# Kernel tuning notes

Measured on AMD Instinct MI355X. Metric: run time of the kernel, lower is better.

The kernel has to match this reference:

```python
import jax, jax.numpy as jnp
import numpy as np
from jax import lax

HEADS = 8
DIM_HEAD = 8
SCALE = DIM_HEAD ** (-0.5)
UP = 64  # nn.Upsample(scale_factor=64), nearest


def _conv_s8(x, w, b):
    # Conv2d(inner, inner, 11x11, stride 8, padding 2) + exact GELU
    y = lax.conv_general_dilated(x, w, window_strides=(8, 8),
                                 padding=((2, 2), (2, 2)),
                                 dimension_numbers=('NCHW', 'OIHW', 'NCHW'))
    return jax.nn.gelu(y + b[None, :, None, None], approximate=False)


def setup_inputs() -> dict:
    key = jax.random.key(0)
    ks = jax.random.split(key, 8)
    b, c, h, w = 2, 64, 48, 48
    inner = HEADS * DIM_HEAD  # 64
    f = jax.random.normal(ks[0], (b, c, h, w), jnp.float32)
    w_qkv = jax.random.normal(ks[1], (inner * 3, c, 1, 1), jnp.float32) * 0.05
    wq = jax.random.normal(ks[2], (inner, inner, 11, 11), jnp.float32) * 0.02
    bq = jax.random.normal(ks[3], (inner,), jnp.float32) * 0.02
    wk = jax.random.normal(ks[4], (inner, inner, 11, 11), jnp.float32) * 0.02
    bk = jax.random.normal(ks[5], (inner,), jnp.float32) * 0.02
    pos_h = jax.random.normal(ks[6], (DIM_HEAD, h), jnp.float32) * SCALE
    pos_w = jax.random.normal(ks[7], (DIM_HEAD, w), jnp.float32) * SCALE
    return {"f": f, "w_qkv": w_qkv, "wq": wq, "bq": bq, "wk": wk,
            "bk": bk, "pos_h": pos_h, "pos_w": pos_w}


def reference(f, w_qkv, wq, bq, wk, bk, pos_h, pos_w):
    b, c, h, w = f.shape
    inner = HEADS * DIM_HEAD
    # 1x1 conv to qkv
    qkv = jnp.einsum('oc,bchw->bohw', w_qkv[:, :, 0, 0], f)
    q, k, v = jnp.split(qkv, 3, axis=1)  # each [b, inner, h, w]
    # positional logits from pre-conv q
    q_full = q.reshape(b, HEADS, DIM_HEAD, h * w)
    emb = (pos_h[:, :, None] + pos_w[:, None, :]).reshape(DIM_HEAD, h * w)
    pos_logits = jnp.einsum('bhci,cj->bhij', q_full, emb)  # [b,H,hw,hw]
    # strided conv + gelu on q,k
    qd = _conv_s8(q, wq, bq)
    kd = _conv_s8(k, wk, bk)
    m = qd.shape[-1]  # downsampled side
    qd = qd.reshape(b, HEADS, DIM_HEAD, m * m) * SCALE
    kd = kd.reshape(b, HEADS, DIM_HEAD, m * m)
    vv = v.reshape(b, HEADS, DIM_HEAD, h * w)
    dots = jnp.einsum('bhci,bhcj->bhij', qd, kd)  # [b,H,m^2,m^2]
    # nearest upsample x64 on last two dims
    dots = jnp.repeat(jnp.repeat(dots, UP, axis=-2), UP, axis=-1)
    attn = jax.nn.softmax(dots + pos_logits, axis=-1)
    fmap = jnp.einsum('bhij,bhcj->bhci', attn, vv)
    return fmap.reshape(b, inner, h, w)
```

## Files before the change

kernel.cpp:

```cpp
#include <hip/hip_runtime.h>
#include <math.h>

#define HW 2304
#define O192 192
#define SCALE_F 0.35355339059327373f

typedef unsigned int u32;
typedef __attribute__((address_space(1))) const u32 gu32;
typedef __attribute__((address_space(3))) u32 lu32;
__device__ __forceinline__ void dma16(const void* g, void* l) {
  __builtin_amdgcn_global_load_lds((gu32*)g, (lu32*)l, 16, 0, 0);
}

__global__ __launch_bounds__(256) void qkv_kernel(
    const float* __restrict__ F, const float* __restrict__ W,
    float* __restrict__ QKV, float* __restrict__ V2) {
  __shared__ __align__(16) float sW[384];
  int blk = blockIdx.x;
  int idx0 = blk * 256;
  int r0 = idx0 / HW;
  int r1 = (idx0 + 255) / HW;
  int tid = threadIdx.x;
  if (tid < 192) {
    int g = tid >> 6, c = tid & 63;
    sW[tid]       = W[((r0 & 63) + g * 64) * 64 + c];
    sW[192 + tid] = W[((r1 & 63) + g * 64) * 64 + c];
  }
  __syncthreads();
  int idx = idx0 + tid;
  int p  = idx % HW;
  int r  = idx / HW;
  int o0 = r & 63;
  int b  = r >> 6;
  const float4* w4 = (const float4*)(sW + ((r == r0) ? 0 : 192));
  const float* f = F + (b * 64) * HW + p;
  float aq = 0.f, ak = 0.f, av = 0.f;
  #pragma unroll 4
  for (int c4 = 0; c4 < 16; c4++) {
    float4 wq = w4[c4];
    float4 wk = w4[16 + c4];
    float4 wv = w4[32 + c4];
    float f0 = f[(c4 * 4 + 0) * HW];
    float f1 = f[(c4 * 4 + 1) * HW];
    float f2 = f[(c4 * 4 + 2) * HW];
    float f3 = f[(c4 * 4 + 3) * HW];
    aq = fmaf(wq.x, f0, aq); ak = fmaf(wk.x, f0, ak); av = fmaf(wv.x, f0, av);
    aq = fmaf(wq.y, f1, aq); ak = fmaf(wk.y, f1, ak); av = fmaf(wv.y, f1, av);
    aq = fmaf(wq.z, f2, aq); ak = fmaf(wk.z, f2, ak); av = fmaf(wv.z, f2, av);
    aq = fmaf(wq.w, f3, aq); ak = fmaf(wk.w, f3, ak); av = fmaf(wv.w, f3, av);
  }
  float* qp = QKV + (b * HW + p) * O192;
  qp[o0]      = aq;
  qp[o0 + 64] = ak;
  V2[(((b << 3) + (o0 >> 3)) * HW + p) * 8 + (o0 & 7)] = av;
}

__global__ __launch_bounds__(256) void conv_kernel(
    const float* __restrict__ QKV, const float* __restrict__ Wq,
    const float* __restrict__ Bq, const float* __restrict__ Wk,
    const float* __restrict__ Bk, float* __restrict__ QD) {
  __shared__ float sW[7744];
  __shared__ float sRed[4 * 64 * 6];
  int blk = blockIdx.x;
  int xcd = blk & 7;
  int T = xcd >> 2, b = (xcd >> 1) & 1, s = xcd & 1;
  int idx = (blk >> 3) * 2 + s;
  int o  = idx / 6;
  int oy = idx % 6;
  const float* Wg = T ? Wk : Wq;
  for (int i = threadIdx.x; i < 7744; i += 256) sW[i] = Wg[o * 7744 + i];
  __syncthreads();
  int wv = threadIdx.x >> 6;
  int c  = threadIdx.x & 63;
  const float* base = QKV + b * (HW * O192) + T * 64 + c;
  float acc[6];
  #pragma unroll
  for (int ox = 0; ox < 6; ox++) acc[ox] = 0.f;
  for (int kyi = 0; kyi < 3; kyi++) {
    int ky = wv * 3 + kyi;
    if (ky > 10) break;
    int y = oy * 8 - 2 + ky;
    if ((unsigned)y < 48u) {
      float xrow[48];
      #pragma unroll
      for (int x = 0; x < 48; x++) xrow[x] = base[(y * 48 + x) * O192];
      #pragma unroll
      for (int kx = 0; kx < 11; kx++) {
        float wt = sW[c * 121 + ky * 11 + kx];
        #pragma unroll
        for (int ox = 0; ox < 6; ox++) {
          int x = ox * 8 - 2 + kx;
          if (x >= 0 && x < 48) acc[ox] = fmaf(xrow[x], wt, acc[ox]);
        }
      }
    }
  }
  #pragma unroll
  for (int ox = 0; ox < 6; ox++) sRed[(wv * 64 + c) * 6 + ox] = acc[ox];
  __syncthreads();
  if (threadIdx.x < 64) {
    int t = threadIdx.x;
    float r[6];
    #pragma unroll
    for (int ox = 0; ox < 6; ox++)
      r[ox] = sRed[t * 6 + ox] + sRed[(64 + t) * 6 + ox]
            + sRed[(128 + t) * 6 + ox] + sRed[(192 + t) * 6 + ox];
    #pragma unroll
    for (int off = 32; off; off >>= 1) {
      #pragma unroll
      for (int ox = 0; ox < 6; ox++) r[ox] += __shfl_down(r[ox], off, 64);
    }
    if (t == 0) {
      float bias = T ? Bk[o] : Bq[o];
      #pragma unroll
      for (int ox = 0; ox < 6; ox++) {
        float g = r[ox] + bias;
        float ge = 0.5f * g * (1.0f + erff(g * 0.70710678118654752f));
        QD[((T * 2 + b) * 64 + o) * 36 + oy * 6 + ox] = ge;
      }
    }
  }
}

#define OFF_V   0
#define OFF_EA  4608
#define OFF_PHT 7680
#define OFF_PWT 8064
#define OFF_E4  8448
#define OFF_U   8592
#define SBUF_N  11152

__global__ __launch_bounds__(512, 4) void attn_kernel(
    const float* __restrict__ QKV, const float* __restrict__ V2,
    const float* __restrict__ QD, const float* __restrict__ PH,
    const float* __restrict__ PW, float* __restrict__ Pnum,
    float* __restrict__ PZ) {
  __shared__ __align__(16) float sB[SBUF_N];
  int blk = blockIdx.x;
  int bh = blk / 36;
  int rem = blk - bh * 36;
  int q = rem & 3, S = rem >> 2;
  int b = bh >> 3, h = bh & 7;
  int tid = threadIdx.x;
  int w = tid >> 6, lane = tid & 63;
  int l32 = lane & 31, chalf = lane >> 5;
  if (tid < 384) {
    sB[OFF_PHT + tid] = PH[(tid & 7) * 48 + (tid >> 3)];
    sB[OFF_PWT + tid] = PW[(tid & 7) * 48 + (tid >> 3)];
  }
  if (tid < 144) {
    int J = tid >> 2, k4 = tid & 3;
    const float* qd = QD + ((0 + b) * 64 + h * 8) * 36 + (S * 4 + k4);
    const float* kd = QD + ((2 + b) * 64 + h * 8) * 36 + J;
    float acc = 0.f;
    #pragma unroll
    for (int c8 = 0; c8 < 8; c8++) acc = fmaf(qd[c8 * 36], kd[c8 * 36], acc);
    sB[OFF_E4 + J * 4 + k4] = __expf(SCALE_F * acc);
  }
  {
    int row = tid >> 1, half = tid & 1;
    *(float4*)(sB + OFF_U + tid * 4) =
      *(const float4*)(QKV + (b * HW + S * 256 + row) * O192 + h * 8 + half * 4);
  }
  {
    const char* src = (const char*)(V2 + (size_t)bh * (HW * 8) + q * 4608);
    for (int m = w; m < 18; m += 8)
      dma16(src + m * 1024 + lane * 16, (char*)(sB + OFF_V) + m * 1024);
  }
  __syncthreads();
  #pragma unroll
  for (int m = 0; m < 6; m++) {
    int flat = tid + m * 512;
    int jyL = flat >> 8, row = flat & 255;
    const float* qp = sB + OFF_U + row * 8;
    const float* pp = sB + OFF_PHT + (q * 12 + jyL) * 8;
    float d = qp[0]*pp[0]+qp[1]*pp[1]+qp[2]*pp[2]+qp[3]*pp[3]
            + qp[4]*pp[4]+qp[5]*pp[5]+qp[6]*pp[6]+qp[7]*pp[7];
    sB[OFF_EA + jyL * 256 + (row & 31) * 8 + (row >> 5)] = __expf(d);
  }
  float pw[6][8];
  #pragma unroll
  for (int i = 0; i < 6; i++) {
    float4 a = *(const float4*)(sB + OFF_PWT + (w * 6 + i) * 8);
    float4 c = *(const float4*)(sB + OFF_PWT + (w * 6 + i) * 8 + 4);
    pw[i][0]=a.x; pw[i][1]=a.y; pw[i][2]=a.z; pw[i][3]=a.w;
    pw[i][4]=c.x; pw[i][5]=c.y; pw[i][6]=c.z; pw[i][7]=c.w;
  }
  float eB[8][6];
  #pragma unroll
  for (int k8 = 0; k8 < 8; k8++) {
    const float* qp = sB + OFF_U + (k8 * 32 + l32) * 8;
    float4 qa = *(const float4*)qp;
    float4 qb = *(const float4*)(qp + 4);
    #pragma unroll
    for (int i = 0; i < 6; i++) {
      float d = qa.x*pw[i][0]+qa.y*pw[i][1]+qa.z*pw[i][2]+qa.w*pw[i][3]
              + qb.x*pw[i][4]+qb.y*pw[i][5]+qb.z*pw[i][6]+qb.w*pw[i][7];
      eB[k8][i] = __expf(d);
    }
  }
  float accv[8][4], zz[8];
  #pragma unroll
  for (int k8 = 0; k8 < 8; k8++) {
    zz[k8] = 0.f;
    #pragma unroll
    for (int c = 0; c < 4; c++) accv[k8][c] = 0.f;
  }
  __syncthreads();
  const float4* sV4 = (const float4*)(sB + OFF_V);
  for (int jyL = 0; jyL < 12; jyL++) {
    float4 ea0 = *(const float4*)(sB + OFF_EA + jyL * 256 + l32 * 8);
    float4 ea1 = *(const float4*)(sB + OFF_EA + jyL * 256 + l32 * 8 + 4);
    int cb = (q * 12 + jyL) * 48 + w * 6;
    int J0 = cb >> 6, J1 = (cb + 5) >> 6;
    int ib = 64 - (cb & 63);
    float4 e0 = *(const float4*)(sB + OFF_E4 + J0 * 4);
    float4 e1 = *(const float4*)(sB + OFF_E4 + J1 * 4);
    float a0[8], a1[8];
    a0[0]=ea0.x*e0.x; a0[1]=ea0.y*e0.x; a0[2]=ea0.z*e0.y; a0[3]=ea0.w*e0.y;
    a0[4]=ea1.x*e0.z; a0[5]=ea1.y*e0.z; a0[6]=ea1.z*e0.w; a0[7]=ea1.w*e0.w;
    a1[0]=ea0.x*e1.x; a1[1]=ea0.y*e1.x; a1[2]=ea0.z*e1.y; a1[3]=ea0.w*e1.y;
    a1[4]=ea1.x*e1.z; a1[5]=ea1.y*e1.z; a1[6]=ea1.z*e1.w; a1[7]=ea1.w*e1.w;
    #pragma unroll
    for (int i = 0; i < 6; i++) {
      float4 v = sV4[(jyL * 48 + w * 6 + i) * 2 + chalf];
      bool s0 = (i < ib);
      #pragma unroll
      for (int k8 = 0; k8 < 8; k8++) {
        float wgt = (s0 ? a0[k8] : a1[k8]) * eB[k8][i];
        accv[k8][0] = fmaf(wgt, v.x, accv[k8][0]);
        accv[k8][1] = fmaf(wgt, v.y, accv[k8][1]);
        accv[k8][2] = fmaf(wgt, v.z, accv[k8][2]);
        accv[k8][3] = fmaf(wgt, v.w, accv[k8][3]);
        zz[k8] += wgt;
      }
    }
  }
  float* sU = sB + OFF_U;
  #pragma unroll
  for (int k8 = 0; k8 < 8; k8++) {
    __syncthreads();
    {
      float* rp = sU + (w * 64 + lane) * 5;
      rp[0] = accv[k8][0]; rp[1] = accv[k8][1];
      rp[2] = accv[k8][2]; rp[3] = accv[k8][3];
      rp[4] = zz[k8];
    }
    __syncthreads();
    if (tid < 256) {
      int row32 = tid & 31, c = tid >> 5;
      int ln = row32 + (c >> 2) * 32;
      float num = 0.f;
      #pragma unroll
      for (int ww = 0; ww < 8; ww++) num += sU[(ww * 64 + ln) * 5 + (c & 3)];
      Pnum[((q * 16 + bh) * 8 + c) * HW + S * 256 + k8 * 32 + row32] = num;
    } else if (tid < 288) {
      int row32 = tid & 31;
      float z = 0.f;
      #pragma unroll
      for (int ww = 0; ww < 8; ww++)
        z += sU[(ww * 64 + row32) * 5 + 4] + sU[(ww * 64 + 32 + row32) * 5 + 4];
      PZ[(q * 16 + bh) * HW + S * 256 + k8 * 32 + row32] = z * 0.5f;
    }
  }
}

__global__ __launch_bounds__(256) void combine_kernel(
    const float* __restrict__ Pnum, const float* __restrict__ PZ,
    float* __restrict__ out) {
  int t = blockIdx.x * 256 + threadIdx.x;
  int row = t % HW;
  int rc = t / HW;
  int c = rc & 7, bh = rc >> 3;
  float num = 0.f, z = 0.f;
  #pragma unroll
  for (int q = 0; q < 4; q++) {
    num += Pnum[((q * 16 + bh) * 8 + c) * HW + row];
    z   += PZ[(q * 16 + bh) * HW + row];
  }
  int b = bh >> 3, h = bh & 7;
  out[(b * 64 + h * 8 + c) * HW + row] = num / z;
}

extern "C" void kernel_launch(void* const* d_in, const int* in_sizes, int n_in,
                              void* d_out, int out_size, void* d_ws, size_t ws_size,
                              hipStream_t stream) {
  const float* F    = (const float*)d_in[0];
  const float* Wqkv = (const float*)d_in[1];
  const float* Wq   = (const float*)d_in[2];
  const float* Bq   = (const float*)d_in[3];
  const float* Wk   = (const float*)d_in[4];
  const float* Bk   = (const float*)d_in[5];
  const float* PH   = (const float*)d_in[6];
  const float* PW   = (const float*)d_in[7];
  float* out = (float*)d_out;

  float* ws   = (float*)d_ws;
  float* QKV  = ws;
  float* V2   = QKV + 2 * HW * O192;
  float* QD   = V2 + 2 * 8 * HW * 8;
  float* Pnum = QD + 2 * 2 * 64 * 36;
  float* PZ   = Pnum + 4 * 16 * 8 * HW;

  qkv_kernel    <<<1152, 256, 0, stream>>>(F, Wqkv, QKV, V2);
  conv_kernel   <<<1536, 256, 0, stream>>>(QKV, Wq, Bq, Wk, Bk, QD);
  attn_kernel   <<<576,  512, 0, stream>>>(QKV, V2, QD, PH, PW, Pnum, PZ);
  combine_kernel<<<1152, 256, 0, stream>>>(Pnum, PZ, out);
}
```

Before: 159.5 us.

## Fuse combine into attention kernel by looping over all key quarters per block

Each attention block now covers 128 query rows across all four key quarters, streaming the V quarters through shared memory in a loop. This removes the Pnum/PZ partial buffers and the separate combine kernel, so normalization is written directly to the output. In exchange the grid shrinks from 576 to 288 blocks with fewer query rows per block, which lowers parallelism on the GPU. The V loads are now serialized between barriers with no double buffering.

```diff
diff --git a/kernel.cpp b/kernel.cpp
--- a/kernel.cpp
+++ b/kernel.cpp
@@ -122,25 +122,26 @@
   }
 }
 
-#define OFF_V   0
-#define OFF_EA  4608
-#define OFF_PHT 7680
-#define OFF_PWT 8064
-#define OFF_E4  8448
-#define OFF_U   8592
-#define SBUF_N  11152
-
-__global__ __launch_bounds__(512, 4) void attn_kernel(
+#define OFF_V    0
+#define OFF_QLO  4608
+#define OFF_QHI  5120
+#define OFF_EA   5632
+#define OFF_PHT  11776
+#define OFF_PWT  12160
+#define OFF_E    12544
+#define OFF_Z    12616
+#define SBUF_N   12648
+
+__global__ __launch_bounds__(512) void attn_kernel(
     const float* __restrict__ QKV, const float* __restrict__ V2,
     const float* __restrict__ QD, const float* __restrict__ PH,
-    const float* __restrict__ PW, float* __restrict__ Pnum,
-    float* __restrict__ PZ) {
+    const float* __restrict__ PW, float* __restrict__ out) {
   __shared__ __align__(16) float sB[SBUF_N];
   int blk = blockIdx.x;
-  int bh = blk / 36;
-  int rem = blk - bh * 36;
-  int q = rem & 3, S = rem >> 2;
+  int bh = blk & 15;
+  int Ip = blk >> 4;
   int b = bh >> 3, h = bh & 7;
+  int r0 = Ip * 128;
   int tid = threadIdx.x;
   int w = tid >> 6, lane = tid & 63;
   int l32 = lane & 31, chalf = lane >> 5;
@@ -148,97 +149,95 @@
     sB[OFF_PHT + tid] = PH[(tid & 7) * 48 + (tid >> 3)];
     sB[OFF_PWT + tid] = PW[(tid & 7) * 48 + (tid >> 3)];
   }
-  if (tid < 144) {
-    int J = tid >> 2, k4 = tid & 3;
-    const float* qd = QD + ((0 + b) * 64 + h * 8) * 36 + (S * 4 + k4);
+  if (tid < 72) {
+    int Ik = tid / 36, J = tid - Ik * 36;
+    const float* qd = QD + ((0 + b) * 64 + h * 8) * 36 + (Ip * 2 + Ik);
     const float* kd = QD + ((2 + b) * 64 + h * 8) * 36 + J;
     float acc = 0.f;
     #pragma unroll
     for (int c8 = 0; c8 < 8; c8++) acc = fmaf(qd[c8 * 36], kd[c8 * 36], acc);
-    sB[OFF_E4 + J * 4 + k4] = __expf(SCALE_F * acc);
-  }
-  {
+    sB[OFF_E + tid] = __expf(SCALE_F * acc);
+  }
+  if (tid < 256) {
     int row = tid >> 1, half = tid & 1;
-    *(float4*)(sB + OFF_U + tid * 4) =
-      *(const float4*)(QKV + (b * HW + S * 256 + row) * O192 + h * 8 + half * 4);
-  }
-  {
-    const char* src = (const char*)(V2 + (size_t)bh * (HW * 8) + q * 4608);
-    for (int m = w; m < 18; m += 8)
-      dma16(src + m * 1024 + lane * 16, (char*)(sB + OFF_V) + m * 1024);
-  }
-  __syncthreads();
-  #pragma unroll
-  for (int m = 0; m < 6; m++) {
+    int slot = (row & 31) * 4 + (row >> 5);
+    float4 qv = *(const float4*)(QKV + (b * HW + r0 + row) * O192 + h * 8 + half * 4);
+    *(float4*)(sB + (half ? OFF_QHI : OFF_QLO) + slot * 4) = qv;
+  }
+  __syncthreads();
+  #pragma unroll
+  for (int m = 0; m < 12; m++) {
     int flat = tid + m * 512;
-    int jyL = flat >> 8, row = flat & 255;
-    const float* qp = sB + OFF_U + row * 8;
-    const float* pp = sB + OFF_PHT + (q * 12 + jyL) * 8;
-    float d = qp[0]*pp[0]+qp[1]*pp[1]+qp[2]*pp[2]+qp[3]*pp[3]
-            + qp[4]*pp[4]+qp[5]*pp[5]+qp[6]*pp[6]+qp[7]*pp[7];
-    sB[OFF_EA + jyL * 256 + (row & 31) * 8 + (row >> 5)] = __expf(d);
-  }
-  float pw[6][8];
-  #pragma unroll
-  for (int i = 0; i < 6; i++) {
-    float4 a = *(const float4*)(sB + OFF_PWT + (w * 6 + i) * 8);
-    float4 c = *(const float4*)(sB + OFF_PWT + (w * 6 + i) * 8 + 4);
-    pw[i][0]=a.x; pw[i][1]=a.y; pw[i][2]=a.z; pw[i][3]=a.w;
-    pw[i][4]=c.x; pw[i][5]=c.y; pw[i][6]=c.z; pw[i][7]=c.w;
-  }
-  float eB[8][6];
-  #pragma unroll
-  for (int k8 = 0; k8 < 8; k8++) {
-    const float* qp = sB + OFF_U + (k8 * 32 + l32) * 8;
-    float4 qa = *(const float4*)qp;
-    float4 qb = *(const float4*)(qp + 4);
+    int jy = flat >> 7, s = flat & 127;
+    float4 qa = *(const float4*)(sB + OFF_QLO + s * 4);
+    float4 qb = *(const float4*)(sB + OFF_QHI + s * 4);
+    const float* pp = sB + OFF_PHT + jy * 8;
+    float d = qa.x*pp[0]+qa.y*pp[1]+qa.z*pp[2]+qa.w*pp[3]
+            + qb.x*pp[4]+qb.y*pp[5]+qb.z*pp[6]+qb.w*pp[7];
+    sB[OFF_EA + flat] = __expf(d);
+  }
+  float eB[4][6];
+  #pragma unroll
+  for (int k8 = 0; k8 < 4; k8++) {
+    float4 qa = *(const float4*)(sB + OFF_QLO + (l32 * 4 + k8) * 4);
+    float4 qb = *(const float4*)(sB + OFF_QHI + (l32 * 4 + k8) * 4);
     #pragma unroll
     for (int i = 0; i < 6; i++) {
-      float d = qa.x*pw[i][0]+qa.y*pw[i][1]+qa.z*pw[i][2]+qa.w*pw[i][3]
-              + qb.x*pw[i][4]+qb.y*pw[i][5]+qb.z*pw[i][6]+qb.w*pw[i][7];
+      const float* pp = sB + OFF_PWT + (w * 6 + i) * 8;
+      float d = qa.x*pp[0]+qa.y*pp[1]+qa.z*pp[2]+qa.w*pp[3]
+              + qb.x*pp[4]+qb.y*pp[5]+qb.z*pp[6]+qb.w*pp[7];
       eB[k8][i] = __expf(d);
     }
   }
-  float accv[8][4], zz[8];
-  #pragma unroll
-  for (int k8 = 0; k8 < 8; k8++) {
+  float accv[4][4], zz[4];
+  #pragma unroll
+  for (int k8 = 0; k8 < 4; k8++) {
     zz[k8] = 0.f;
     #pragma unroll
     for (int c = 0; c < 4; c++) accv[k8][c] = 0.f;
   }
-  __syncthreads();
   const float4* sV4 = (const float4*)(sB + OFF_V);
-  for (int jyL = 0; jyL < 12; jyL++) {
-    float4 ea0 = *(const float4*)(sB + OFF_EA + jyL * 256 + l32 * 8);
-    float4 ea1 = *(const float4*)(sB + OFF_EA + jyL * 256 + l32 * 8 + 4);
-    int cb = (q * 12 + jyL) * 48 + w * 6;
-    int J0 = cb >> 6, J1 = (cb + 5) >> 6;
-    int ib = 64 - (cb & 63);
-    float4 e0 = *(const float4*)(sB + OFF_E4 + J0 * 4);
-    float4 e1 = *(const float4*)(sB + OFF_E4 + J1 * 4);
-    float a0[8], a1[8];
-    a0[0]=ea0.x*e0.x; a0[1]=ea0.y*e0.x; a0[2]=ea0.z*e0.y; a0[3]=ea0.w*e0.y;
-    a0[4]=ea1.x*e0.z; a0[5]=ea1.y*e0.z; a0[6]=ea1.z*e0.w; a0[7]=ea1.w*e0.w;
-    a1[0]=ea0.x*e1.x; a1[1]=ea0.y*e1.x; a1[2]=ea0.z*e1.y; a1[3]=ea0.w*e1.y;
-    a1[4]=ea1.x*e1.z; a1[5]=ea1.y*e1.z; a1[6]=ea1.z*e1.w; a1[7]=ea1.w*e1.w;
-    #pragma unroll
-    for (int i = 0; i < 6; i++) {
-      float4 v = sV4[(jyL * 48 + w * 6 + i) * 2 + chalf];
-      bool s0 = (i < ib);
-      #pragma unroll
-      for (int k8 = 0; k8 < 8; k8++) {
-        float wgt = (s0 ? a0[k8] : a1[k8]) * eB[k8][i];
-        accv[k8][0] = fmaf(wgt, v.x, accv[k8][0]);
-        accv[k8][1] = fmaf(wgt, v.y, accv[k8][1]);
-        accv[k8][2] = fmaf(wgt, v.z, accv[k8][2]);
-        accv[k8][3] = fmaf(wgt, v.w, accv[k8][3]);
-        zz[k8] += wgt;
+  for (int p = 0; p < 4; p++) {
+    __syncthreads();
+    {
+      const char* src = (const char*)(V2 + (size_t)bh * (HW * 8) + p * 4608);
+      for (int m = w; m < 18; m += 8)
+        dma16(src + m * 1024 + lane * 16, (char*)(sB + OFF_V) + m * 1024);
+    }
+    __syncthreads();
+    #pragma unroll
+    for (int jyL = 0; jyL < 12; jyL++) {
+      int jy = p * 12 + jyL;
+      float4 ea = *(const float4*)(sB + OFF_EA + jy * 128 + l32 * 4);
+      int cb = jy * 48 + w * 6;
+      int J0 = cb >> 6, J1 = (cb + 5) >> 6;
+      int ib = 64 - (cb & 63);
+      float e00 = sB[OFF_E + J0], e01 = sB[OFF_E + 36 + J0];
+      float e10 = sB[OFF_E + J1], e11 = sB[OFF_E + 36 + J1];
+      float a0[4], a1[4];
+      a0[0] = ea.x * e00; a0[1] = ea.y * e00;
+      a0[2] = ea.z * e01; a0[3] = ea.w * e01;
+      a1[0] = ea.x * e10; a1[1] = ea.y * e10;
+      a1[2] = ea.z * e11; a1[3] = ea.w * e11;
+      #pragma unroll
+      for (int i = 0; i < 6; i++) {
+        float4 v = sV4[(jyL * 48 + w * 6 + i) * 2 + chalf];
+        bool s0 = (i < ib);
+        #pragma unroll
+        for (int k8 = 0; k8 < 4; k8++) {
+          float wgt = (s0 ? a0[k8] : a1[k8]) * eB[k8][i];
+          accv[k8][0] = fmaf(wgt, v.x, accv[k8][0]);
+          accv[k8][1] = fmaf(wgt, v.y, accv[k8][1]);
+          accv[k8][2] = fmaf(wgt, v.z, accv[k8][2]);
+          accv[k8][3] = fmaf(wgt, v.w, accv[k8][3]);
+          zz[k8] += wgt;
+        }
       }
     }
   }
-  float* sU = sB + OFF_U;
-  #pragma unroll
-  for (int k8 = 0; k8 < 8; k8++) {
+  float* sU = sB + OFF_EA;
+  #pragma unroll
+  for (int k8 = 0; k8 < 4; k8++) {
     __syncthreads();
     {
       float* rp = sU + (w * 64 + lane) * 5;
@@ -247,39 +246,24 @@
       rp[4] = zz[k8];
     }
     __syncthreads();
+    if (tid < 32) {
+      float z = 0.f;
+      #pragma unroll
+      for (int ww = 0; ww < 8; ww++)
+        z += sU[(ww * 64 + tid) * 5 + 4] + sU[(ww * 64 + 32 + tid) * 5 + 4];
+      sB[OFF_Z + tid] = 2.0f / z;
+    }
+    __syncthreads();
     if (tid < 256) {
       int row32 = tid & 31, c = tid >> 5;
-      int ln = row32 + (c >> 2) * 32;
+      int ln = ((c >> 2) << 5) + row32;
       float num = 0.f;
       #pragma unroll
       for (int ww = 0; ww < 8; ww++) num += sU[(ww * 64 + ln) * 5 + (c & 3)];
-      Pnum[((q * 16 + bh) * 8 + c) * HW + S * 256 + k8 * 32 + row32] = num;
-    } else if (tid < 288) {
-      int row32 = tid & 31;
-      float z = 0.f;
-      #pragma unroll
-      for (int ww = 0; ww < 8; ww++)
-        z += sU[(ww * 64 + row32) * 5 + 4] + sU[(ww * 64 + 32 + row32) * 5 + 4];
-      PZ[(q * 16 + bh) * HW + S * 256 + k8 * 32 + row32] = z * 0.5f;
-    }
-  }
-}
-
-__global__ __launch_bounds__(256) void combine_kernel(
-    const float* __restrict__ Pnum, const float* __restrict__ PZ,
-    float* __restrict__ out) {
-  int t = blockIdx.x * 256 + threadIdx.x;
-  int row = t % HW;
-  int rc = t / HW;
-  int c = rc & 7, bh = rc >> 3;
-  float num = 0.f, z = 0.f;
-  #pragma unroll
-  for (int q = 0; q < 4; q++) {
-    num += Pnum[((q * 16 + bh) * 8 + c) * HW + row];
-    z   += PZ[(q * 16 + bh) * HW + row];
-  }
-  int b = bh >> 3, h = bh & 7;
-  out[(b * 64 + h * 8 + c) * HW + row] = num / z;
+      out[(b * 64 + h * 8 + c) * HW + r0 + k8 * 32 + row32] =
+          num * sB[OFF_Z + row32];
+    }
+  }
 }
 
 extern "C" void kernel_launch(void* const* d_in, const int* in_sizes, int n_in,
@@ -295,15 +279,12 @@
   const float* PW   = (const float*)d_in[7];
   float* out = (float*)d_out;
 
-  float* ws   = (float*)d_ws;
-  float* QKV  = ws;
-  float* V2   = QKV + 2 * HW * O192;
-  float* QD   = V2 + 2 * 8 * HW * 8;
-  float* Pnum = QD + 2 * 2 * 64 * 36;
-  float* PZ   = Pnum + 4 * 16 * 8 * HW;
-
-  qkv_kernel    <<<1152, 256, 0, stream>>>(F, Wqkv, QKV, V2);
-  conv_kernel   <<<1536, 256, 0, stream>>>(QKV, Wq, Bq, Wk, Bk, QD);
-  attn_kernel   <<<576,  512, 0, stream>>>(QKV, V2, QD, PH, PW, Pnum, PZ);
-  combine_kernel<<<1152, 256, 0, stream>>>(Pnum, PZ, out);
-}
+  float* ws  = (float*)d_ws;
+  float* QKV = ws;
+  float* V2  = QKV + 2 * HW * O192;
+  float* QD  = V2 + 2 * 8 * HW * 8;
+
+  qkv_kernel <<<1152, 256, 0, stream>>>(F, Wqkv, QKV, V2);
+  conv_kernel<<<1536, 256, 0, stream>>>(QKV, Wq, Bq, Wk, Bk, QD);
+  attn_kernel<<<288,  512, 0, stream>>>(QKV, V2, QD, PH, PW, out);
+}
```

Result: no change. 159.6 us (+0.1%).
